# Kernel tuning notes

Hardware: AMD Instinct MI355X
Metric: run time of the kernel (lower is better)

## Reference

```python
import jax, jax.numpy as jnp
import numpy as np
from math import factorial

P = 3          # polynomial order
D_I = 4096     # sketch output dim per order
C = 512        # input channels
B, H, W = 8, 28, 28
GAMMA = 1e-4


def setup_inputs() -> dict:
    key = jax.random.key(0)
    k1, k2, k3 = jax.random.split(key, 3)
    x = jax.random.normal(k1, (B, H, W, C), dtype=jnp.float32)
    # AlphaInitializer: alpha_i = sqrt(exp(-2g) * (2g)^i / i!)
    gam2 = np.full(P + 1, 2.0 * GAMMA)
    numer = np.power(gam2, np.arange(P + 1))
    denom = np.array([factorial(i) for i in range(P + 1)], dtype=np.float64)
    alpha = jnp.asarray(np.sqrt(np.exp(-gam2) * numer / denom), dtype=jnp.float32)
    # count-sketch hash indices and sign bits, one pair per order t in [0, p)
    h_idx = jax.random.randint(k2, (P, C), 0, D_I)
    s_bits = jax.random.randint(k3, (P, C), 0, 2).astype(jnp.int32)
    return {"x": x, "alpha": alpha, "h_idx": h_idx, "s_bits": s_bits}


def reference(x, alpha, h_idx, s_bits):
    Bs, Hs, Ws, Ch = x.shape
    p = h_idx.shape[0]
    d_i = D_I
    signs = (2 * s_bits - 1).astype(x.dtype)          # (p, C) in {-1,+1}
    x_flat = x.reshape(-1, Ch)                        # (B*H*W, C)

    def count_sketch(h, s):
        # scatter-add channels into d_i buckets: equivalent to x_flat @ S
        return jnp.zeros((x_flat.shape[0], d_i), x.dtype).at[:, h].add(x_flat * s)

    sk = jax.vmap(count_sketch)(h_idx, signs)         # (p, N, d_i)
    xs = jnp.transpose(sk, (1, 0, 2)).reshape(Bs, Hs * Ws, p, d_i)

    xf = jnp.fft.fft(xs.astype(jnp.complex64), axis=-1)
    cp = jnp.cumprod(xf, axis=-2)[:, :, 1:, :]        # orders 2..p
    xi = jnp.real(jnp.fft.ifft(cp, axis=-1)).mean(axis=1)   # (B, p-1, d_i)

    x_p = xi * alpha[2:].reshape(1, p - 1, 1)
    zeroth = alpha[0] * jnp.ones((Bs, 1), x.dtype)
    first = alpha[1] * x.mean(axis=(1, 2))            # (B, C)
    phi = jnp.concatenate([zeroth, first, x_p.reshape(Bs, -1)], axis=-1)
    phi = jnp.sign(phi) * jnp.sqrt(jnp.abs(phi) + 1e-12)    # signed sqrt
    return phi / jnp.linalg.norm(phi, axis=-1, keepdims=True)
```

## Files before the change

### kernel.cpp

```cpp
#include <hip/hip_runtime.h>

#define BATCH 8
#define NPOS 784
#define CH 512
#define DI 4096
#define CHUNKS 98
#define PPC 8
#define PHI_LEN 8705
#define S_FLOATS (BATCH * 2 * 2049 * 2)
#define PHI_OFF S_FLOATS

__device__ __forceinline__ float2 cmul(float2 a, float2 b) {
  return make_float2(a.x * b.x - a.y * b.y, a.x * b.y + a.y * b.x);
}

__device__ __forceinline__ void dft4(float2& a, float2& b, float2& c, float2& d) {
  float t0x = a.x + c.x, t0y = a.y + c.y;
  float t1x = a.x - c.x, t1y = a.y - c.y;
  float t2x = b.x + d.x, t2y = b.y + d.y;
  float t3x = b.x - d.x, t3y = b.y - d.y;
  a = make_float2(t0x + t2x, t0y + t2y);
  c = make_float2(t0x - t2x, t0y - t2y);
  b = make_float2(t1x + t3y, t1y - t3x);
  d = make_float2(t1x - t3y, t1y + t3x);
}

__device__ __forceinline__ void dft16(float2 v[16]) {
  dft4(v[0], v[4], v[8], v[12]);
  dft4(v[1], v[5], v[9], v[13]);
  dft4(v[2], v[6], v[10], v[14]);
  dft4(v[3], v[7], v[11], v[15]);
  const float C1 = 0.92387953251128674f, S1 = 0.38268343236508977f;
  const float R = 0.70710678118654752f;
  v[5]  = cmul(v[5],  make_float2( C1, -S1));
  v[9]  = cmul(v[9],  make_float2(  R,  -R));
  v[13] = cmul(v[13], make_float2( S1, -C1));
  v[6]  = cmul(v[6],  make_float2(  R,  -R));
  v[10] = cmul(v[10], make_float2(0.f, -1.f));
  v[14] = cmul(v[14], make_float2( -R,  -R));
  v[7]  = cmul(v[7],  make_float2( S1, -C1));
  v[11] = cmul(v[11], make_float2( -R,  -R));
  v[15] = cmul(v[15], make_float2(-C1,  S1));
  dft4(v[0], v[1], v[2], v[3]);
  dft4(v[4], v[5], v[6], v[7]);
  dft4(v[8], v[9], v[10], v[11]);
  dft4(v[12], v[13], v[14], v[15]);
}

__device__ __forceinline__ void twiddle16(float2 v[16], float2 w) {
  float2 w2 = cmul(w, w);
  float2 w3 = cmul(w2, w);
  float2 w4 = cmul(w2, w2);
  float2 w5 = cmul(w3, w2);
  float2 w6 = cmul(w3, w3);
  float2 w7 = cmul(w4, w3);
  float2 w8 = cmul(w4, w4);
  float2 w9 = cmul(w5, w4);
  float2 w10 = cmul(w5, w5);
  float2 w11 = cmul(w6, w5);
  float2 w12 = cmul(w6, w6);
  float2 w13 = cmul(w7, w6);
  float2 w14 = cmul(w7, w7);
  float2 w15 = cmul(w8, w7);
  v[1] = cmul(v[1], w);    v[2] = cmul(v[2], w2);   v[3] = cmul(v[3], w3);
  v[4] = cmul(v[4], w4);   v[5] = cmul(v[5], w5);   v[6] = cmul(v[6], w6);
  v[7] = cmul(v[7], w7);   v[8] = cmul(v[8], w8);   v[9] = cmul(v[9], w9);
  v[10] = cmul(v[10], w10); v[11] = cmul(v[11], w11); v[12] = cmul(v[12], w12);
  v[13] = cmul(v[13], w13); v[14] = cmul(v[14], w14); v[15] = cmul(v[15], w15);
}

__device__ __forceinline__ void fft_stages(float2* Z, int tid, float2 w1b,
                                           float2 w2b) {
  const int tl = tid & 15;
  const int g16 = tid << 4;
  const int b1 = (tid >> 4) << 8;
  const int base2 = (tid & 240) | (tl ^ ((tid >> 4) & 15));
  __syncthreads();
  {
    float2 v[16];
    #pragma unroll
    for (int u = 0; u < 16; ++u) v[u] = Z[g16 + (u ^ tl)];
    dft16(v);
    #pragma unroll
    for (int k = 0; k < 16; ++k)
      Z[g16 + (k ^ tl)] = v[(k >> 2) + ((k & 3) << 2)];
  }
  __syncthreads();
  {
    float2 v[16];
    #pragma unroll
    for (int u = 0; u < 16; ++u) v[u] = Z[b1 + (u << 4) + (tl ^ u)];
    twiddle16(v, w1b);
    dft16(v);
    #pragma unroll
    for (int k = 0; k < 16; ++k)
      Z[b1 + (k << 4) + (tl ^ k)] = v[(k >> 2) + ((k & 3) << 2)];
  }
  __syncthreads();
  {
    float2 v[16];
    #pragma unroll
    for (int u = 0; u < 16; ++u) v[u] = Z[(u << 8) + base2];
    twiddle16(v, w2b);
    dft16(v);
    #pragma unroll
    for (int k = 0; k < 16; ++k)
      Z[(k << 8) + base2] = v[(k >> 2) + ((k & 3) << 2)];
  }
  __syncthreads();
}

__global__ __launch_bounds__(256) void cbp_stage1(
    const float* __restrict__ x, const float* __restrict__ alpha,
    const int* __restrict__ h_idx, const int* __restrict__ s_bits,
    float* __restrict__ ws) {
  __shared__ float2 Z[DI];
  float* Zf = (float*)Z;
  const int tid = threadIdx.x;
  const int bb = blockIdx.x / CHUNKS;
  const int ch = blockIdx.x % CHUNKS;

  auto mapidx = [](int h) {
    int r = ((h & 15) << 8) | (h & 240) | (h >> 8);
    return r ^ ((r >> 4) & 15);
  };
  const int c0 = tid * 2, c1 = c0 + 1;
  const int h0a = mapidx(h_idx[c0]);
  const int h0b = mapidx(h_idx[c1]);
  const int h1a = mapidx(h_idx[CH + c0]);
  const int h1b = mapidx(h_idx[CH + c1]);
  const int h2a = mapidx(h_idx[2 * CH + c0]);
  const int h2b = mapidx(h_idx[2 * CH + c1]);
  const float s0a = (float)(2 * s_bits[c0] - 1);
  const float s0b = (float)(2 * s_bits[c1] - 1);
  const float s1a = (float)(2 * s_bits[CH + c0] - 1);
  const float s1b = (float)(2 * s_bits[CH + c1] - 1);
  const float s2a = (float)(2 * s_bits[2 * CH + c0] - 1);
  const float s2b = (float)(2 * s_bits[2 * CH + c1] - 1);

  const int tl = tid & 15;
  const int base2 = (tid & 240) | (tl ^ ((tid >> 4) & 15));
  float sv, cv;
  __sincosf(-2.4543692606170259e-2f * (float)tl, &sv, &cv);
  const float2 w1b = make_float2(cv, sv);
  __sincosf(-1.5339807878856412e-3f * (float)tid, &sv, &cv);
  const float2 w2b = make_float2(cv, sv);

  float2 acc2[8], acc3[8], p2e[8], p2o[8];
  #pragma unroll
  for (int j = 0; j < 8; ++j) {
    acc2[j] = make_float2(0.f, 0.f);
    acc3[j] = make_float2(0.f, 0.f);
  }
  float acc2x = 0.f, acc3x = 0.f, p2xe = 0.f, p2xo = 0.f;
  float xsa = 0.f, xsb = 0.f;

  #pragma unroll
  for (int q = 0; q < 16; ++q) Z[tid + (q << 8)] = make_float2(0.f, 0.f);
  __syncthreads();

  for (int ip = 0; ip < 4; ++ip) {
    const int n0 = bb * NPOS + ch * PPC + ip * 2;
    const float2 xv0 = *(const float2*)(x + (size_t)n0 * CH + c0);
    const float2 xv1 = *(const float2*)(x + (size_t)(n0 + 1) * CH + c0);
    xsa += xv0.x + xv1.x;
    xsb += xv0.y + xv1.y;

    atomicAdd(&Zf[2 * h0a], xv0.x * s0a);
    atomicAdd(&Zf[2 * h0b], xv0.y * s0b);
    atomicAdd(&Zf[2 * h1a + 1], xv0.x * s1a);
    atomicAdd(&Zf[2 * h1b + 1], xv0.y * s1b);
    fft_stages(Z, tid, w1b, w2b);
    #pragma unroll
    for (int jj = 0; jj < 8; ++jj) {
      const int k = tid + (jj << 8);
      const int ak = (jj << 8) + base2;
      const int m = (DI - k) & (DI - 1);
      const int am = m ^ ((m >> 4) & 15);
      float2 Zk = Z[ak], Zm = Z[am];
      Z[ak] = make_float2(0.f, 0.f);
      Z[am] = make_float2(0.f, 0.f);
      float2 X0 = make_float2(0.5f * (Zk.x + Zm.x), 0.5f * (Zk.y - Zm.y));
      float2 X1 = make_float2(0.5f * (Zk.y + Zm.y), -0.5f * (Zk.x - Zm.x));
      float2 P2 = cmul(X0, X1);
      p2e[jj] = P2;
      acc2[jj].x += P2.x;
      acc2[jj].y += P2.y;
    }
    if (tid == 0) {
      float2 Zq = Z[2048];
      Z[2048] = make_float2(0.f, 0.f);
      p2xe = Zq.x * Zq.y;
      acc2x += p2xe;
    }
    __syncthreads();

    atomicAdd(&Zf[2 * h0a], xv1.x * s0a);
    atomicAdd(&Zf[2 * h0b], xv1.y * s0b);
    atomicAdd(&Zf[2 * h1a + 1], xv1.x * s1a);
    atomicAdd(&Zf[2 * h1b + 1], xv1.y * s1b);
    fft_stages(Z, tid, w1b, w2b);
    #pragma unroll
    for (int jj = 0; jj < 8; ++jj) {
      const int k = tid + (jj << 8);
      const int ak = (jj << 8) + base2;
      const int m = (DI - k) & (DI - 1);
      const int am = m ^ ((m >> 4) & 15);
      float2 Zk = Z[ak], Zm = Z[am];
      Z[ak] = make_float2(0.f, 0.f);
      Z[am] = make_float2(0.f, 0.f);
      float2 X0 = make_float2(0.5f * (Zk.x + Zm.x), 0.5f * (Zk.y - Zm.y));
      float2 X1 = make_float2(0.5f * (Zk.y + Zm.y), -0.5f * (Zk.x - Zm.x));
      float2 P2 = cmul(X0, X1);
      p2o[jj] = P2;
      acc2[jj].x += P2.x;
      acc2[jj].y += P2.y;
    }
    if (tid == 0) {
      float2 Zq = Z[2048];
      Z[2048] = make_float2(0.f, 0.f);
      p2xo = Zq.x * Zq.y;
      acc2x += p2xo;
    }
    __syncthreads();

    atomicAdd(&Zf[2 * h2a], xv0.x * s2a);
    atomicAdd(&Zf[2 * h2a + 1], xv1.x * s2a);
    atomicAdd(&Zf[2 * h2b], xv0.y * s2b);
    atomicAdd(&Zf[2 * h2b + 1], xv1.y * s2b);
    fft_stages(Z, tid, w1b, w2b);
    #pragma unroll
    for (int jj = 0; jj < 8; ++jj) {
      const int k = tid + (jj << 8);
      const int ak = (jj << 8) + base2;
      const int m = (DI - k) & (DI - 1);
      const int am = m ^ ((m >> 4) & 15);
      float2 Zk = Z[ak], Zm = Z[am];
      Z[ak] = make_float2(0.f, 0.f);
      Z[am] = make_float2(0.f, 0.f);
      float2 Xa = make_float2(0.5f * (Zk.x + Zm.x), 0.5f * (Zk.y - Zm.y));
      float2 Xb = make_float2(0.5f * (Zk.y + Zm.y), -0.5f * (Zk.x - Zm.x));
      float2 Pa = cmul(p2e[jj], Xa);
      float2 Pb = cmul(p2o[jj], Xb);
      acc3[jj].x += Pa.x + Pb.x;
      acc3[jj].y += Pa.y + Pb.y;
    }
    if (tid == 0) {
      float2 Zq = Z[2048];
      Z[2048] = make_float2(0.f, 0.f);
      acc3x += p2xe * Zq.x + p2xo * Zq.y;
    }
    __syncthreads();
  }

  float* S = ws;
  #pragma unroll
  for (int jj = 0; jj < 8; ++jj) {
    const int k = tid + (jj << 8);
    float* p2p = S + ((size_t)(bb * 2 + 0) * 2049 + k) * 2;
    atomicAdd(p2p, acc2[jj].x);
    atomicAdd(p2p + 1, acc2[jj].y);
    float* p3p = S + ((size_t)(bb * 2 + 1) * 2049 + k) * 2;
    atomicAdd(p3p, acc3[jj].x);
    atomicAdd(p3p + 1, acc3[jj].y);
  }
  if (tid == 0) {
    atomicAdd(S + ((size_t)(bb * 2 + 0) * 2049 + 2048) * 2, acc2x);
    atomicAdd(S + ((size_t)(bb * 2 + 1) * 2049 + 2048) * 2, acc3x);
  }

  const float sc1 = alpha[1] * (1.0f / (float)NPOS);
  float* phi = ws + PHI_OFF;
  atomicAdd(&phi[(size_t)bb * PHI_LEN + 1 + c0], xsa * sc1);
  atomicAdd(&phi[(size_t)bb * PHI_LEN + 1 + c1], xsb * sc1);
}

__device__ inline void fft4096_r2(float2* Z, const float2* W, int tid) {
  for (int s = 1; s <= 12; ++s) {
    __syncthreads();
    const int half = 1 << (s - 1);
    const int tsh = 12 - s;
    #pragma unroll
    for (int q = 0; q < 8; ++q) {
      int bidx = tid + q * 256;
      int j = bidx & (half - 1);
      int i1 = ((bidx >> (s - 1)) << s) + j;
      int i2 = i1 + half;
      float2 w = W[j << tsh];
      float2 u = Z[i1];
      float2 v = Z[i2];
      float2 t = cmul(w, v);
      Z[i1] = make_float2(u.x + t.x, u.y + t.y);
      Z[i2] = make_float2(u.x - t.x, u.y - t.y);
    }
  }
  __syncthreads();
}

__global__ __launch_bounds__(256) void cbp_stage2(
    const float* __restrict__ ws_in, const float* __restrict__ alpha,
    float* __restrict__ ws_phi) {
  __shared__ float2 Z[DI];
  __shared__ float2 W[DI / 2];
  const int tid = threadIdx.x;

  for (int r = tid; r < DI / 2; r += 256) {
    float ang = 1.5339807878856412e-3f * (float)r;
    float sv, cv;
    sincosf(ang, &sv, &cv);
    W[r] = make_float2(cv, sv);
  }

  const int b = blockIdx.x >> 1;
  const int t = blockIdx.x & 1;
  const float* Sp = ws_in + (size_t)(b * 2 + t) * 2049 * 2;

  for (int k = tid; k <= 2048; k += 256) {
    float re = Sp[k * 2];
    float im = Sp[k * 2 + 1];
    Z[__brev((unsigned)k) >> 20] = make_float2(re, im);
    if (k > 0 && k < 2048) {
      Z[__brev((unsigned)(DI - k)) >> 20] = make_float2(re, -im);
    }
  }
  fft4096_r2(Z, W, tid);

  const float scale = alpha[2 + t] / ((float)DI * (float)NPOS);
  float* out = ws_phi + (size_t)b * PHI_LEN + 513 + t * DI;
  for (int d = tid; d < DI; d += 256) out[d] = Z[d].x * scale;
}

__global__ __launch_bounds__(256) void cbp_stage3(
    const float* __restrict__ ws_phi, const float* __restrict__ alpha,
    float* __restrict__ out) {
  __shared__ float red[4];
  const int b = blockIdx.x;
  const int tid = threadIdx.x;
  const float* pr = ws_phi + (size_t)b * PHI_LEN;
  const float a0 = alpha[0];

  float w[35];
  float ssum = 0.f;
  #pragma unroll
  for (int j = 0; j < 35; ++j) {
    const int idx = tid + j * 256;
    float wv = 0.f;
    if (idx < PHI_LEN) {
      float v = (idx == 0) ? a0 : pr[idx];
      float sq = sqrtf(fabsf(v) + 1e-12f);
      wv = (v > 0.f) ? sq : ((v < 0.f) ? -sq : 0.f);
    }
    w[j] = wv;
    ssum += wv * wv;
  }
  for (int off = 32; off > 0; off >>= 1) ssum += __shfl_down(ssum, off);
  if ((tid & 63) == 0) red[tid >> 6] = ssum;
  __syncthreads();
  const float tot = red[0] + red[1] + red[2] + red[3];
  const float inv = 1.0f / sqrtf(tot);

  #pragma unroll
  for (int j = 0; j < 35; ++j) {
    const int idx = tid + j * 256;
    if (idx < PHI_LEN) out[(size_t)b * PHI_LEN + idx] = w[j] * inv;
  }
}

extern "C" void kernel_launch(void* const* d_in, const int* in_sizes, int n_in,
                              void* d_out, int out_size, void* d_ws,
                              size_t ws_size, hipStream_t stream) {
  const float* x = (const float*)d_in[0];
  const float* alpha = (const float*)d_in[1];
  const int* h_idx = (const int*)d_in[2];
  const int* s_bits = (const int*)d_in[3];
  float* out = (float*)d_out;
  float* ws = (float*)d_ws;

  const size_t zero_bytes = (size_t)(S_FLOATS + BATCH * PHI_LEN) * sizeof(float);
  hipMemsetAsync(d_ws, 0, zero_bytes, stream);

  cbp_stage1<<<dim3(BATCH * CHUNKS), dim3(256), 0, stream>>>(x, alpha, h_idx,
                                                             s_bits, ws);
  cbp_stage2<<<dim3(BATCH * 2), dim3(256), 0, stream>>>(ws, alpha,
                                                        ws + PHI_OFF);
  cbp_stage3<<<dim3(BATCH), dim3(256), 0, stream>>>(ws + PHI_OFF, alpha, out);
}
```

Before: 258.7 us.

## Re-pair sketch FFT slots to cut carried registers and halve positions per block

Reorganizes how the three order sketches for two positions are packed into the real/imag halves of the three complex FFTs. Only one carried array is kept instead of two product arrays, which lowers register pressure, and launch bounds now request 4 blocks per SIMD. Positions per block drop from 8 to 4, doubling the grid but also doubling the global atomic reductions. It also folds the sign into a sign bit of the packed hash index and computes twiddle powers with fewer chained multiplies.

```diff
diff --git a/kernel.cpp b/kernel.cpp
--- a/kernel.cpp
+++ b/kernel.cpp
@@ -4,8 +4,8 @@
 #define NPOS 784
 #define CH 512
 #define DI 4096
-#define CHUNKS 98
-#define PPC 8
+#define PPC 4
+#define CHUNKS (NPOS / PPC)
 #define PHI_LEN 8705
 #define S_FLOATS (BATCH * 2 * 2049 * 2)
 #define PHI_OFF S_FLOATS
@@ -51,22 +51,23 @@
   float2 w2 = cmul(w, w);
   float2 w3 = cmul(w2, w);
   float2 w4 = cmul(w2, w2);
-  float2 w5 = cmul(w3, w2);
-  float2 w6 = cmul(w3, w3);
-  float2 w7 = cmul(w4, w3);
   float2 w8 = cmul(w4, w4);
-  float2 w9 = cmul(w5, w4);
-  float2 w10 = cmul(w5, w5);
-  float2 w11 = cmul(w6, w5);
-  float2 w12 = cmul(w6, w6);
-  float2 w13 = cmul(w7, w6);
-  float2 w14 = cmul(w7, w7);
-  float2 w15 = cmul(w8, w7);
-  v[1] = cmul(v[1], w);    v[2] = cmul(v[2], w2);   v[3] = cmul(v[3], w3);
-  v[4] = cmul(v[4], w4);   v[5] = cmul(v[5], w5);   v[6] = cmul(v[6], w6);
-  v[7] = cmul(v[7], w7);   v[8] = cmul(v[8], w8);   v[9] = cmul(v[9], w9);
-  v[10] = cmul(v[10], w10); v[11] = cmul(v[11], w11); v[12] = cmul(v[12], w12);
-  v[13] = cmul(v[13], w13); v[14] = cmul(v[14], w14); v[15] = cmul(v[15], w15);
+  float2 w12 = cmul(w8, w4);
+  v[1] = cmul(v[1], w);
+  v[2] = cmul(v[2], w2);
+  v[3] = cmul(v[3], w3);
+  v[4] = cmul(v[4], w4);
+  v[5] = cmul(v[5], cmul(w4, w));
+  v[6] = cmul(v[6], cmul(w4, w2));
+  v[7] = cmul(v[7], cmul(w4, w3));
+  v[8] = cmul(v[8], w8);
+  v[9] = cmul(v[9], cmul(w8, w));
+  v[10] = cmul(v[10], cmul(w8, w2));
+  v[11] = cmul(v[11], cmul(w8, w3));
+  v[12] = cmul(v[12], w12);
+  v[13] = cmul(v[13], cmul(w12, w));
+  v[14] = cmul(v[14], cmul(w12, w2));
+  v[15] = cmul(v[15], cmul(w12, w3));
 }
 
 __device__ __forceinline__ void fft_stages(float2* Z, int tid, float2 w1b,
@@ -110,7 +111,7 @@
   __syncthreads();
 }
 
-__global__ __launch_bounds__(256) void cbp_stage1(
+__global__ __launch_bounds__(256, 4) void cbp_stage1(
     const float* __restrict__ x, const float* __restrict__ alpha,
     const int* __restrict__ h_idx, const int* __restrict__ s_bits,
     float* __restrict__ ws) {
@@ -120,56 +121,53 @@
   const int bb = blockIdx.x / CHUNKS;
   const int ch = blockIdx.x % CHUNKS;
 
-  auto mapidx = [](int h) {
+  auto mapq = [](int h, int s) {
     int r = ((h & 15) << 8) | (h & 240) | (h >> 8);
-    return r ^ ((r >> 4) & 15);
+    return (r ^ ((r >> 4) & 15)) | ((s ^ 1) << 31);
+  };
+  auto sgn = [](float v, int p) {
+    return __int_as_float(__float_as_int(v) ^ (p & 0x80000000u));
   };
   const int c0 = tid * 2, c1 = c0 + 1;
-  const int h0a = mapidx(h_idx[c0]);
-  const int h0b = mapidx(h_idx[c1]);
-  const int h1a = mapidx(h_idx[CH + c0]);
-  const int h1b = mapidx(h_idx[CH + c1]);
-  const int h2a = mapidx(h_idx[2 * CH + c0]);
-  const int h2b = mapidx(h_idx[2 * CH + c1]);
-  const float s0a = (float)(2 * s_bits[c0] - 1);
-  const float s0b = (float)(2 * s_bits[c1] - 1);
-  const float s1a = (float)(2 * s_bits[CH + c0] - 1);
-  const float s1b = (float)(2 * s_bits[CH + c1] - 1);
-  const float s2a = (float)(2 * s_bits[2 * CH + c0] - 1);
-  const float s2b = (float)(2 * s_bits[2 * CH + c1] - 1);
+  const int q0a = mapq(h_idx[c0], s_bits[c0]);
+  const int q0b = mapq(h_idx[c1], s_bits[c1]);
+  const int q1a = mapq(h_idx[CH + c0], s_bits[CH + c0]);
+  const int q1b = mapq(h_idx[CH + c1], s_bits[CH + c1]);
+  const int q2a = mapq(h_idx[2 * CH + c0], s_bits[2 * CH + c0]);
+  const int q2b = mapq(h_idx[2 * CH + c1], s_bits[2 * CH + c1]);
 
   const int tl = tid & 15;
   const int base2 = (tid & 240) | (tl ^ ((tid >> 4) & 15));
-  float sv, cv;
-  __sincosf(-2.4543692606170259e-2f * (float)tl, &sv, &cv);
-  const float2 w1b = make_float2(cv, sv);
-  __sincosf(-1.5339807878856412e-3f * (float)tid, &sv, &cv);
-  const float2 w2b = make_float2(cv, sv);
-
-  float2 acc2[8], acc3[8], p2e[8], p2o[8];
+  float sv_, cv_;
+  __sincosf(-2.4543692606170259e-2f * (float)tl, &sv_, &cv_);
+  const float2 w1b = make_float2(cv_, sv_);
+  __sincosf(-1.5339807878856412e-3f * (float)tid, &sv_, &cv_);
+  const float2 w2b = make_float2(cv_, sv_);
+
+  float2 acc2[8], acc3[8], carry[8];
   #pragma unroll
   for (int j = 0; j < 8; ++j) {
     acc2[j] = make_float2(0.f, 0.f);
     acc3[j] = make_float2(0.f, 0.f);
   }
-  float acc2x = 0.f, acc3x = 0.f, p2xe = 0.f, p2xo = 0.f;
+  float acc2x = 0.f, acc3x = 0.f, carryx = 0.f;
   float xsa = 0.f, xsb = 0.f;
 
   #pragma unroll
   for (int q = 0; q < 16; ++q) Z[tid + (q << 8)] = make_float2(0.f, 0.f);
   __syncthreads();
 
-  for (int ip = 0; ip < 4; ++ip) {
+  for (int ip = 0; ip < PPC / 2; ++ip) {
     const int n0 = bb * NPOS + ch * PPC + ip * 2;
     const float2 xv0 = *(const float2*)(x + (size_t)n0 * CH + c0);
     const float2 xv1 = *(const float2*)(x + (size_t)(n0 + 1) * CH + c0);
     xsa += xv0.x + xv1.x;
     xsb += xv0.y + xv1.y;
 
-    atomicAdd(&Zf[2 * h0a], xv0.x * s0a);
-    atomicAdd(&Zf[2 * h0b], xv0.y * s0b);
-    atomicAdd(&Zf[2 * h1a + 1], xv0.x * s1a);
-    atomicAdd(&Zf[2 * h1b + 1], xv0.y * s1b);
+    atomicAdd(&Zf[2 * (q0a & 0xFFF)], sgn(xv0.x, q0a));
+    atomicAdd(&Zf[2 * (q0b & 0xFFF)], sgn(xv0.y, q0b));
+    atomicAdd(&Zf[2 * (q1a & 0xFFF) + 1], sgn(xv0.x, q1a));
+    atomicAdd(&Zf[2 * (q1b & 0xFFF) + 1], sgn(xv0.y, q1b));
     fft_stages(Z, tid, w1b, w2b);
     #pragma unroll
     for (int jj = 0; jj < 8; ++jj) {
@@ -180,25 +178,25 @@
       float2 Zk = Z[ak], Zm = Z[am];
       Z[ak] = make_float2(0.f, 0.f);
       Z[am] = make_float2(0.f, 0.f);
-      float2 X0 = make_float2(0.5f * (Zk.x + Zm.x), 0.5f * (Zk.y - Zm.y));
-      float2 X1 = make_float2(0.5f * (Zk.y + Zm.y), -0.5f * (Zk.x - Zm.x));
-      float2 P2 = cmul(X0, X1);
-      p2e[jj] = P2;
-      acc2[jj].x += P2.x;
-      acc2[jj].y += P2.y;
+      float2 E = make_float2(0.5f * (Zk.x + Zm.x), 0.5f * (Zk.y - Zm.y));
+      float2 O = make_float2(0.5f * (Zk.y + Zm.y), -0.5f * (Zk.x - Zm.x));
+      float2 P = cmul(E, O);
+      carry[jj] = P;
+      acc2[jj].x += P.x;
+      acc2[jj].y += P.y;
     }
     if (tid == 0) {
       float2 Zq = Z[2048];
       Z[2048] = make_float2(0.f, 0.f);
-      p2xe = Zq.x * Zq.y;
-      acc2x += p2xe;
+      carryx = Zq.x * Zq.y;
+      acc2x += carryx;
     }
     __syncthreads();
 
-    atomicAdd(&Zf[2 * h0a], xv1.x * s0a);
-    atomicAdd(&Zf[2 * h0b], xv1.y * s0b);
-    atomicAdd(&Zf[2 * h1a + 1], xv1.x * s1a);
-    atomicAdd(&Zf[2 * h1b + 1], xv1.y * s1b);
+    atomicAdd(&Zf[2 * (q2a & 0xFFF)], sgn(xv0.x, q2a));
+    atomicAdd(&Zf[2 * (q2b & 0xFFF)], sgn(xv0.y, q2b));
+    atomicAdd(&Zf[2 * (q0a & 0xFFF) + 1], sgn(xv1.x, q0a));
+    atomicAdd(&Zf[2 * (q0b & 0xFFF) + 1], sgn(xv1.y, q0b));
     fft_stages(Z, tid, w1b, w2b);
     #pragma unroll
     for (int jj = 0; jj < 8; ++jj) {
@@ -209,25 +207,25 @@
       float2 Zk = Z[ak], Zm = Z[am];
       Z[ak] = make_float2(0.f, 0.f);
       Z[am] = make_float2(0.f, 0.f);
-      float2 X0 = make_float2(0.5f * (Zk.x + Zm.x), 0.5f * (Zk.y - Zm.y));
-      float2 X1 = make_float2(0.5f * (Zk.y + Zm.y), -0.5f * (Zk.x - Zm.x));
-      float2 P2 = cmul(X0, X1);
-      p2o[jj] = P2;
-      acc2[jj].x += P2.x;
-      acc2[jj].y += P2.y;
+      float2 E = make_float2(0.5f * (Zk.x + Zm.x), 0.5f * (Zk.y - Zm.y));
+      float2 O = make_float2(0.5f * (Zk.y + Zm.y), -0.5f * (Zk.x - Zm.x));
+      float2 P3 = cmul(carry[jj], E);
+      acc3[jj].x += P3.x;
+      acc3[jj].y += P3.y;
+      carry[jj] = O;
     }
     if (tid == 0) {
       float2 Zq = Z[2048];
       Z[2048] = make_float2(0.f, 0.f);
-      p2xo = Zq.x * Zq.y;
-      acc2x += p2xo;
+      acc3x += carryx * Zq.x;
+      carryx = Zq.y;
     }
     __syncthreads();
 
-    atomicAdd(&Zf[2 * h2a], xv0.x * s2a);
-    atomicAdd(&Zf[2 * h2a + 1], xv1.x * s2a);
-    atomicAdd(&Zf[2 * h2b], xv0.y * s2b);
-    atomicAdd(&Zf[2 * h2b + 1], xv1.y * s2b);
+    atomicAdd(&Zf[2 * (q1a & 0xFFF)], sgn(xv1.x, q1a));
+    atomicAdd(&Zf[2 * (q1b & 0xFFF)], sgn(xv1.y, q1b));
+    atomicAdd(&Zf[2 * (q2a & 0xFFF) + 1], sgn(xv1.x, q2a));
+    atomicAdd(&Zf[2 * (q2b & 0xFFF) + 1], sgn(xv1.y, q2b));
     fft_stages(Z, tid, w1b, w2b);
     #pragma unroll
     for (int jj = 0; jj < 8; ++jj) {
@@ -238,17 +236,21 @@
       float2 Zk = Z[ak], Zm = Z[am];
       Z[ak] = make_float2(0.f, 0.f);
       Z[am] = make_float2(0.f, 0.f);
-      float2 Xa = make_float2(0.5f * (Zk.x + Zm.x), 0.5f * (Zk.y - Zm.y));
-      float2 Xb = make_float2(0.5f * (Zk.y + Zm.y), -0.5f * (Zk.x - Zm.x));
-      float2 Pa = cmul(p2e[jj], Xa);
-      float2 Pb = cmul(p2o[jj], Xb);
-      acc3[jj].x += Pa.x + Pb.x;
-      acc3[jj].y += Pa.y + Pb.y;
+      float2 E = make_float2(0.5f * (Zk.x + Zm.x), 0.5f * (Zk.y - Zm.y));
+      float2 O = make_float2(0.5f * (Zk.y + Zm.y), -0.5f * (Zk.x - Zm.x));
+      float2 P = cmul(carry[jj], E);
+      acc2[jj].x += P.x;
+      acc2[jj].y += P.y;
+      float2 P3 = cmul(P, O);
+      acc3[jj].x += P3.x;
+      acc3[jj].y += P3.y;
     }
     if (tid == 0) {
       float2 Zq = Z[2048];
       Z[2048] = make_float2(0.f, 0.f);
-      acc3x += p2xe * Zq.x + p2xo * Zq.y;
+      float t = carryx * Zq.x;
+      acc2x += t;
+      acc3x += t * Zq.y;
     }
     __syncthreads();
   }
```

New measurement: 493.1 us. 90.6% more time.
